# Kernel tuning notes

Measured on AMD Instinct MI355X. Metric: run time of the kernel, lower is better.

Reference implementation:

```python
import jax, jax.numpy as jnp
import numpy as np

K = 60
BATCH, NCLS, H, W = 8, 2, 512, 512


def _neighbors(x):
    # x: [B,H,W] int32 in {0,1}. Returns P2..P9 clockwise starting north.
    p = jnp.pad(x, ((0, 0), (1, 1), (1, 1)))
    P2 = p[:, :-2, 1:-1]   # N
    P3 = p[:, :-2, 2:]     # NE
    P4 = p[:, 1:-1, 2:]    # E
    P5 = p[:, 2:, 2:]      # SE
    P6 = p[:, 2:, 1:-1]    # S
    P7 = p[:, 2:, :-2]     # SW
    P8 = p[:, 1:-1, :-2]   # W
    P9 = p[:, :-2, :-2]    # NW
    return P2, P3, P4, P5, P6, P7, P8, P9


def _substep(x, first):
    # One Zhang-Suen thinning sub-iteration (the algorithm used by
    # skimage.morphology.skeletonize for 2D images).
    P2, P3, P4, P5, P6, P7, P8, P9 = _neighbors(x)
    seq = (P2, P3, P4, P5, P6, P7, P8, P9, P2)
    # A = number of 0->1 transitions in circular neighbor sequence
    A = sum(((seq[i] == 0) & (seq[i + 1] == 1)).astype(jnp.int32) for i in range(8))
    Bn = P2 + P3 + P4 + P5 + P6 + P7 + P8 + P9
    if first:
        c3 = P2 * P4 * P6
        c4 = P4 * P6 * P8
    else:
        c3 = P2 * P4 * P8
        c4 = P2 * P6 * P8
    delete = (x == 1) & (Bn >= 2) & (Bn <= 6) & (A == 1) & (c3 == 0) & (c4 == 0)
    return x * (1 - delete.astype(x.dtype))


def _skeletonize(img):
    # img: [B,H,W] int32 binary. Iterate thinning until fixed point.
    def body(state):
        x, _ = state
        x2 = _substep(_substep(x, True), False)
        return x2, jnp.any(x2 != x)

    def cond(state):
        return state[1]

    out, _ = jax.lax.while_loop(cond, body, (img, jnp.array(True)))
    return out


def _conv(x, kernel, pad):
    # x: [B,1,H,W], kernel: [1,1,k,k], 'same' padding pad
    return jax.lax.conv_general_dilated(x, kernel, (1, 1), [(pad, pad), (pad, pad)])


def setup_inputs() -> dict:
    key = jax.random.key(0)
    k1, k2 = jax.random.split(key)
    pred = jax.random.normal(k1, (BATCH, NCLS, H, W), dtype=jnp.float32)
    target = jax.random.randint(k2, (BATCH, H, W), 0, NCLS, dtype=jnp.int32)
    return {"pred": pred, "target": target}


def reference(pred, target):
    # Per-pixel cross entropy, reduction='none'
    logp = jax.nn.log_softmax(pred, axis=1)
    L = -jnp.take_along_axis(logp, target[:, None].astype(jnp.int32), axis=1)[:, 0]  # [B,H,W]

    # Skeletonize the hard prediction (nonzero = foreground)
    A = jnp.argmax(pred, axis=1)
    skel = _skeletonize((A != 0).astype(jnp.int32))  # [B,H,W]
    Bm = skel[:, None].astype(pred.dtype)            # [B,1,H,W]

    # 3x3 neighbor count (center zeroed); endpoints C where product == 1
    k3 = jnp.ones((1, 1, 3, 3), pred.dtype).at[0, 0, 1, 1].set(0.0)
    C = Bm * _conv(Bm, k3, 1)
    C = (C == 1.0).astype(pred.dtype)

    # 9x9 endpoint density, scaled by K; zeros -> weight 1
    k9 = jnp.ones((1, 1, 9, 9), pred.dtype)
    N = _conv(C, k9, 4) * K
    Wmap = N + (N == 0.0).astype(pred.dtype)  # [B,1,H,W]

    return jnp.mean(Wmap[:, 0] * L)
```

## Files before the change

### kernel.cpp

```cpp
#include <hip/hip_runtime.h>

#define BATCH   8
#define HH      512
#define WW      512
#define IMGPIX  (HH * WW)
#define NPIX    (BATCH * IMGPIX)
#define NWORDS  (NPIX / 64)
#define KFAC    60.0f
#define MAX_PAIRS 256
#define WPR     8
#define LDSTR   9
#define FPSCALE 262144.0

typedef unsigned long long u64;
typedef unsigned int u32;

__global__ void prep_kernel(const float* __restrict__ pred, const int* __restrict__ target,
                            float* __restrict__ L, u64* __restrict__ xp,
                            u64* __restrict__ acc64, u32* __restrict__ ticket) {
    int i = blockIdx.x * blockDim.x + threadIdx.x;
    if (i == 0) { acc64[0] = 0ULL; ticket[0] = 0u; }
    if (i >= NPIX) return;
    int b = i >> 18;
    int hw = i & (IMGPIX - 1);
    float p0 = pred[((size_t)(2 * b) << 18) + hw];
    float p1 = pred[((size_t)(2 * b + 1) << 18) + hw];
    float m = fmaxf(p0, p1);
    float lse = m + logf(expf(p0 - m) + expf(p1 - m));
    int t = target[i];
    L[i] = lse - (t ? p1 : p0);
    u64 word = __ballot(p1 > p0);
    if ((threadIdx.x & 63) == 0) xp[i >> 6] = word;
}

#define FA(a,b,c,s,cy) { u64 _x = (a)^(b); (s) = _x^(c); (cy) = ((a)&(b)) | ((c)&_x); }
#define HA(a,b,s,cy)   { (s) = (a)^(b); (cy) = (a)&(b); }

template<int FIRST>
__device__ __forceinline__ u32 zs_substep(u64* __restrict__ img,
                                          const u32* __restrict__ c0,
                                          const u32* __restrict__ c1,
                                          u32* __restrict__ cw, int h)
{
    u32 m = c0[h] | c1[h];
    if (h > 0)      m |= c0[h-1] | c1[h-1];
    if (h < HH-1)   m |= c0[h+1] | c1[h+1];
    u32 active = (m | (m << 1) | (m >> 1)) & 0xFFu;
    u32 loadm  = (active | (active << 1) | (active >> 1)) & 0xFFu;

    u64 U[WPR], M[WPR], D[WPR], nrow[WPR];
    #pragma unroll
    for (int wc = 0; wc < WPR; ++wc) {
        if ((loadm >> wc) & 1) {
            U[wc] = (h > 0)      ? img[(h-1) * LDSTR + wc] : 0ULL;
            M[wc] =                img[h     * LDSTR + wc];
            D[wc] = (h < HH - 1) ? img[(h+1) * LDSTR + wc] : 0ULL;
        } else { U[wc] = 0ULL; M[wc] = 0ULL; D[wc] = 0ULL; }
    }
    __syncthreads();

    u32 chnew = 0;
    #pragma unroll
    for (int wc = 0; wc < WPR; ++wc) {
        if ((active >> wc) & 1) {
            u64 Uc = U[wc], Mc = M[wc], Dc = D[wc];
            u64 Up = wc     ? U[wc-1] : 0ULL;
            u64 Mp = wc     ? M[wc-1] : 0ULL;
            u64 Dp = wc     ? D[wc-1] : 0ULL;
            u64 Un = wc < 7 ? U[wc+1] : 0ULL;
            u64 Mn = wc < 7 ? M[wc+1] : 0ULL;
            u64 Dn = wc < 7 ? D[wc+1] : 0ULL;
            u64 P2 = Uc;
            u64 P6 = Dc;
            u64 P3 = (Uc >> 1) | (Un << 63);
            u64 P4 = (Mc >> 1) | (Mn << 63);
            u64 P5 = (Dc >> 1) | (Dn << 63);
            u64 P9 = (Uc << 1) | (Up >> 63);
            u64 P8 = (Mc << 1) | (Mp >> 63);
            u64 P7 = (Dc << 1) | (Dp >> 63);

            u64 sa,ca, sb,cb, sc,cc, b0,cd, sd,ce, b1,cf, b2,b3;
            FA(P2,P3,P4, sa,ca);
            FA(P5,P6,P7, sb,cb);
            FA(P8,P9,sa, sc,cc);
            HA(sb,sc,    b0,cd);
            FA(ca,cb,cc, sd,ce);
            HA(sd,cd,    b1,cf);
            HA(ce,cf,    b2,b3);
            u64 ge2 = b1 | b2 | b3;
            u64 le6 = ~(b3 | (b0 & b1 & b2));

            u64 e, seen, two = 0;
            seen = (~P2) & P3;
            e = (~P3) & P4; two |= seen & e; seen |= e;
            e = (~P4) & P5; two |= seen & e; seen |= e;
            e = (~P5) & P6; two |= seen & e; seen |= e;
            e = (~P6) & P7; two |= seen & e; seen |= e;
            e = (~P7) & P8; two |= seen & e; seen |= e;
            e = (~P8) & P9; two |= seen & e; seen |= e;
            e = (~P9) & P2; two |= seen & e; seen |= e;
            u64 A1 = seen & ~two;

            u64 c34;
            if (FIRST) { u64 t = P4 & P6; c34 = t & (P2 | P8); }
            else       { u64 t = P2 & P8; c34 = t & (P4 | P6); }

            u64 del = Mc & ge2 & le6 & A1 & ~c34;
            nrow[wc] = Mc ^ del;
            chnew |= (u32)(del != 0ULL) << wc;
        }
    }
    #pragma unroll
    for (int wc = 0; wc < WPR; ++wc)
        if ((active >> wc) & 1) img[h * LDSTR + wc] = nrow[wc];
    cw[h] = chnew;
    return chnew;
}

__global__ __launch_bounds__(512)
void skel_kernel(const u64* __restrict__ xp, u64* __restrict__ eg)
{
    __shared__ u64 img[HH * LDSTR];
    __shared__ u32 chm[2][HH];
    const int b = blockIdx.x;
    const int h = threadIdx.x;

    const u64* src = xp + (size_t)b * (HH * WPR);
    #pragma unroll
    for (int wc = 0; wc < WPR; ++wc) img[h * LDSTR + wc] = src[h * WPR + wc];
    chm[0][h] = 0xFFu; chm[1][h] = 0xFFu;
    __syncthreads();

    for (int p = 0; p < MAX_PAIRS; ++p) {
        u32 ch1 = zs_substep<1>(img, chm[0], chm[1], chm[0], h);
        __syncthreads();
        u32 ch2 = zs_substep<0>(img, chm[0], chm[1], chm[1], h);
        if (!__syncthreads_or((ch1 | ch2) != 0)) break;
    }

    u64 U[WPR], M[WPR], D[WPR];
    #pragma unroll
    for (int wc = 0; wc < WPR; ++wc) {
        U[wc] = (h > 0)      ? img[(h-1) * LDSTR + wc] : 0ULL;
        M[wc] =                img[h     * LDSTR + wc];
        D[wc] = (h < HH - 1) ? img[(h+1) * LDSTR + wc] : 0ULL;
    }
    u64* egr = eg + (size_t)b * (HH * WPR) + (size_t)h * WPR;
    #pragma unroll
    for (int wc = 0; wc < WPR; ++wc) {
        u64 Uc = U[wc], Mc = M[wc], Dc = D[wc];
        u64 Up = wc     ? U[wc-1] : 0ULL;
        u64 Mp = wc     ? M[wc-1] : 0ULL;
        u64 Dp = wc     ? D[wc-1] : 0ULL;
        u64 Un = wc < 7 ? U[wc+1] : 0ULL;
        u64 Mn = wc < 7 ? M[wc+1] : 0ULL;
        u64 Dn = wc < 7 ? D[wc+1] : 0ULL;
        u64 P2 = Uc;
        u64 P6 = Dc;
        u64 P3 = (Uc >> 1) | (Un << 63);
        u64 P4 = (Mc >> 1) | (Mn << 63);
        u64 P5 = (Dc >> 1) | (Dn << 63);
        u64 P9 = (Uc << 1) | (Up >> 63);
        u64 P8 = (Mc << 1) | (Mp >> 63);
        u64 P7 = (Dc << 1) | (Dp >> 63);
        u64 e, seen, two = 0;
        seen = P2;
        e = P3; two |= seen & e; seen |= e;
        e = P4; two |= seen & e; seen |= e;
        e = P5; two |= seen & e; seen |= e;
        e = P6; two |= seen & e; seen |= e;
        e = P7; two |= seen & e; seen |= e;
        e = P8; two |= seen & e; seen |= e;
        e = P9; two |= seen & e; seen |= e;
        egr[wc] = Mc & seen & ~two;
    }
}

struct Planes { u64 p0, p1, p2, p3; };

__device__ __forceinline__ Planes vcount9(const u64 r[9]) {
    u64 s0,c0, s1,c1, s2,c2, p0,t0, t1,t2, p1,t3, p2,p3;
    FA(r[0],r[1],r[2], s0,c0);
    FA(r[3],r[4],r[5], s1,c1);
    FA(r[6],r[7],r[8], s2,c2);
    FA(s0,s1,s2, p0,t0);
    FA(c0,c1,c2, t1,t2);
    HA(t0,t1,    p1,t3);
    HA(t2,t3,    p2,p3);
    Planes P; P.p0 = p0; P.p1 = p1; P.p2 = p2; P.p3 = p3; return P;
}

__device__ __forceinline__ u64 spread8(u64 bb) {
    u64 s = (bb * 0x0101010101010101ULL) & 0x8040201008040201ULL;
    return ((s + 0x7f7f7f7f7f7f7f7fULL) >> 7) & 0x0101010101010101ULL;
}

__device__ __forceinline__ u64 vbytes(const Planes& P, int g) {
    int s = 8 * g;
    return  spread8((P.p0 >> s) & 0xFFULL)
         + (spread8((P.p1 >> s) & 0xFFULL) << 1)
         + (spread8((P.p2 >> s) & 0xFFULL) << 2)
         + (spread8((P.p3 >> s) & 0xFFULL) << 3);
}

__global__ __launch_bounds__(256)
void final_kernel(const float* __restrict__ L, const u64* __restrict__ eg,
                  u64* __restrict__ acc64, u32* __restrict__ ticket,
                  float* __restrict__ out) {
    __shared__ float sm[256];
    int wi = blockIdx.x * blockDim.x + threadIdx.x;
    int b  = wi >> 12;
    int h  = (wi >> 3) & (HH - 1);
    int wc = wi & 7;
    const u64* img = eg + ((size_t)b << 12);

    u64 rows[3][9];
    #pragma unroll
    for (int dh = -4; dh <= 4; ++dh) {
        int hh = h + dh;
        bool okh = (unsigned)hh < (unsigned)HH;
        const u64* rp = img + hh * WPR;
        rows[0][dh + 4] = (okh && wc > 0) ? rp[wc - 1] : 0ULL;
        rows[1][dh + 4] = okh             ? rp[wc]     : 0ULL;
        rows[2][dh + 4] = (okh && wc < 7) ? rp[wc + 1] : 0ULL;
    }
    Planes Pm = vcount9(rows[0]);
    Planes Pc = vcount9(rows[1]);
    Planes Pp = vcount9(rows[2]);

    u64 v[10];
    v[0] = vbytes(Pm, 7);
    #pragma unroll
    for (int g = 0; g < 8; ++g) v[g + 1] = vbytes(Pc, g);
    v[9] = vbytes(Pp, 0);

    const float4* Lr = (const float4*)(L + ((size_t)wi << 6));
    float acc = 0.0f;
    #pragma unroll
    for (int g = 0; g < 8; ++g) {
        u64 a = v[g + 1], lo = v[g], hi = v[g + 2];
        u64 n = a;
        #pragma unroll
        for (int d = 1; d <= 4; ++d) {
            n += (a >> (8 * d)) | (hi << (64 - 8 * d));
            n += (a << (8 * d)) | (lo >> (64 - 8 * d));
        }
        float4 f0 = Lr[2 * g], f1 = Lr[2 * g + 1];
        #pragma unroll
        for (int j = 0; j < 8; ++j) {
            int cnt = (int)((n >> (8 * j)) & 0xFFULL);
            float wgt = cnt ? (float)(60 * cnt) : 1.0f;
            float lv = (j < 4) ? ((j == 0) ? f0.x : (j == 1) ? f0.y : (j == 2) ? f0.z : f0.w)
                               : ((j == 4) ? f1.x : (j == 5) ? f1.y : (j == 6) ? f1.z : f1.w);
            acc += wgt * lv;
        }
    }

    sm[threadIdx.x] = acc;
    __syncthreads();
    for (int s = 128; s > 0; s >>= 1) {
        if (threadIdx.x < s) sm[threadIdx.x] += sm[threadIdx.x + s];
        __syncthreads();
    }
    if (threadIdx.x == 0) {
        u64 vfx = (u64)(long long)llrintf(sm[0] * (float)FPSCALE);
        atomicAdd(acc64, vfx);
        __threadfence();
        u32 t = atomicAdd(ticket, 1u);
        if (t == (u32)(gridDim.x - 1)) {
            __threadfence();
            u64 total = __hip_atomic_load(acc64, __ATOMIC_RELAXED, __HIP_MEMORY_SCOPE_AGENT);
            out[0] = (float)((double)(long long)total / (FPSCALE * (double)NPIX));
        }
    }
}

extern "C" void kernel_launch(void* const* d_in, const int* in_sizes, int n_in,
                              void* d_out, int out_size, void* d_ws, size_t ws_size,
                              hipStream_t stream) {
    const float* pred = (const float*)d_in[0];
    const int* target = (const int*)d_in[1];
    float* out = (float*)d_out;
    char* ws = (char*)d_ws;

    float* L    = (float*)(ws);
    u64* xp     = (u64*)(ws + 8388608);
    u64* eg     = (u64*)(ws + 8650752);
    u64* acc64  = (u64*)(ws + 8912896);
    u32* ticket = (u32*)(ws + 8912904);

    prep_kernel<<<dim3(NPIX / 256), dim3(256), 0, stream>>>(pred, target, L, xp, acc64, ticket);
    skel_kernel<<<dim3(BATCH), dim3(512), 0, stream>>>(xp, eg);
    final_kernel<<<dim3(NWORDS / 256), dim3(256), 0, stream>>>(L, eg, acc64, ticket, out);
}
```

Before: 62.01 us.

## Keep own skeleton row in registers with padded LDS halo rows

Rewrites the thinning loop so each thread keeps its own row in registers and only reloads the neighbouring rows from LDS. It adds zero halo rows so boundary checks disappear. It drops the per-row change-mask activity tracking and instead skips all-zero words and skips the LDS writeback when nothing changed. This trades the earlier sparse-activity skipping for fewer LDS loads, simpler control flow and lower register pressure. Words with foreground but no changes are now always recomputed.

```diff
diff --git a/kernel.cpp b/kernel.cpp
--- a/kernel.cpp
+++ b/kernel.cpp
@@ -6,11 +6,10 @@
 #define IMGPIX  (HH * WW)
 #define NPIX    (BATCH * IMGPIX)
 #define NWORDS  (NPIX / 64)
-#define KFAC    60.0f
-#define MAX_PAIRS 256
 #define WPR     8
 #define LDSTR   9
 #define FPSCALE 262144.0
+#define MAXPAIR 256
 
 typedef unsigned long long u64;
 typedef unsigned int u32;
@@ -37,126 +36,117 @@
 #define HA(a,b,s,cy)   { (s) = (a)^(b); (cy) = (a)&(b); }
 
 template<int FIRST>
-__device__ __forceinline__ u32 zs_substep(u64* __restrict__ img,
-                                          const u32* __restrict__ c0,
-                                          const u32* __restrict__ c1,
-                                          u32* __restrict__ cw, int h)
+__device__ __forceinline__ u64 zs_row(const u64* __restrict__ U, u64* __restrict__ M,
+                                      const u64* __restrict__ D)
 {
-    u32 m = c0[h] | c1[h];
-    if (h > 0)      m |= c0[h-1] | c1[h-1];
-    if (h < HH-1)   m |= c0[h+1] | c1[h+1];
-    u32 active = (m | (m << 1) | (m >> 1)) & 0xFFu;
-    u32 loadm  = (active | (active << 1) | (active >> 1)) & 0xFFu;
-
-    u64 U[WPR], M[WPR], D[WPR], nrow[WPR];
-    #pragma unroll
-    for (int wc = 0; wc < WPR; ++wc) {
-        if ((loadm >> wc) & 1) {
-            U[wc] = (h > 0)      ? img[(h-1) * LDSTR + wc] : 0ULL;
-            M[wc] =                img[h     * LDSTR + wc];
-            D[wc] = (h < HH - 1) ? img[(h+1) * LDSTR + wc] : 0ULL;
-        } else { U[wc] = 0ULL; M[wc] = 0ULL; D[wc] = 0ULL; }
-    }
-    __syncthreads();
-
-    u32 chnew = 0;
-    #pragma unroll
-    for (int wc = 0; wc < WPR; ++wc) {
-        if ((active >> wc) & 1) {
-            u64 Uc = U[wc], Mc = M[wc], Dc = D[wc];
-            u64 Up = wc     ? U[wc-1] : 0ULL;
-            u64 Mp = wc     ? M[wc-1] : 0ULL;
-            u64 Dp = wc     ? D[wc-1] : 0ULL;
-            u64 Un = wc < 7 ? U[wc+1] : 0ULL;
-            u64 Mn = wc < 7 ? M[wc+1] : 0ULL;
-            u64 Dn = wc < 7 ? D[wc+1] : 0ULL;
-            u64 P2 = Uc;
-            u64 P6 = Dc;
-            u64 P3 = (Uc >> 1) | (Un << 63);
-            u64 P4 = (Mc >> 1) | (Mn << 63);
-            u64 P5 = (Dc >> 1) | (Dn << 63);
-            u64 P9 = (Uc << 1) | (Up >> 63);
-            u64 P8 = (Mc << 1) | (Mp >> 63);
-            u64 P7 = (Dc << 1) | (Dp >> 63);
-
-            u64 sa,ca, sb,cb, sc,cc, b0,cd, sd,ce, b1,cf, b2,b3;
-            FA(P2,P3,P4, sa,ca);
-            FA(P5,P6,P7, sb,cb);
-            FA(P8,P9,sa, sc,cc);
-            HA(sb,sc,    b0,cd);
-            FA(ca,cb,cc, sd,ce);
-            HA(sd,cd,    b1,cf);
-            HA(ce,cf,    b2,b3);
-            u64 ge2 = b1 | b2 | b3;
-            u64 le6 = ~(b3 | (b0 & b1 & b2));
-
-            u64 e, seen, two = 0;
-            seen = (~P2) & P3;
-            e = (~P3) & P4; two |= seen & e; seen |= e;
-            e = (~P4) & P5; two |= seen & e; seen |= e;
-            e = (~P5) & P6; two |= seen & e; seen |= e;
-            e = (~P6) & P7; two |= seen & e; seen |= e;
-            e = (~P7) & P8; two |= seen & e; seen |= e;
-            e = (~P8) & P9; two |= seen & e; seen |= e;
-            e = (~P9) & P2; two |= seen & e; seen |= e;
-            u64 A1 = seen & ~two;
-
-            u64 c34;
-            if (FIRST) { u64 t = P4 & P6; c34 = t & (P2 | P8); }
-            else       { u64 t = P2 & P8; c34 = t & (P4 | P6); }
-
-            u64 del = Mc & ge2 & le6 & A1 & ~c34;
-            nrow[wc] = Mc ^ del;
-            chnew |= (u32)(del != 0ULL) << wc;
-        }
-    }
-    #pragma unroll
-    for (int wc = 0; wc < WPR; ++wc)
-        if ((active >> wc) & 1) img[h * LDSTR + wc] = nrow[wc];
-    cw[h] = chnew;
-    return chnew;
+    u64 ch = 0;
+    #pragma unroll
+    for (int k = 0; k < WPR; ++k) {
+        u64 Mc = M[k];
+        if (Mc == 0ULL) continue;
+        u64 Uc = U[k], Dc = D[k];
+        u64 Up = k     ? U[k-1] : 0ULL;
+        u64 Mp = k     ? M[k-1] : 0ULL;
+        u64 Dp = k     ? D[k-1] : 0ULL;
+        u64 Un = k < 7 ? U[k+1] : 0ULL;
+        u64 Mn = k < 7 ? M[k+1] : 0ULL;
+        u64 Dn = k < 7 ? D[k+1] : 0ULL;
+        u64 P2 = Uc, P6 = Dc;
+        u64 P3 = (Uc >> 1) | (Un << 63);
+        u64 P4 = (Mc >> 1) | (Mn << 63);
+        u64 P5 = (Dc >> 1) | (Dn << 63);
+        u64 P9 = (Uc << 1) | (Up >> 63);
+        u64 P8 = (Mc << 1) | (Mp >> 63);
+        u64 P7 = (Dc << 1) | (Dp >> 63);
+
+        u64 sa,ca, sb,cb, sc,cc, b0,cd, sd,ce, b1,cf, b2,b3;
+        FA(P2,P3,P4, sa,ca);
+        FA(P5,P6,P7, sb,cb);
+        FA(P8,P9,sa, sc,cc);
+        HA(sb,sc,    b0,cd);
+        FA(ca,cb,cc, sd,ce);
+        HA(sd,cd,    b1,cf);
+        HA(ce,cf,    b2,b3);
+        u64 ge2 = b1 | b2 | b3;
+        u64 le6 = ~(b3 | (b0 & b1 & b2));
+
+        u64 e, seen, two = 0;
+        seen = (~P2) & P3;
+        e = (~P3) & P4; two |= seen & e; seen |= e;
+        e = (~P4) & P5; two |= seen & e; seen |= e;
+        e = (~P5) & P6; two |= seen & e; seen |= e;
+        e = (~P6) & P7; two |= seen & e; seen |= e;
+        e = (~P7) & P8; two |= seen & e; seen |= e;
+        e = (~P8) & P9; two |= seen & e; seen |= e;
+        e = (~P9) & P2; two |= seen & e; seen |= e;
+        u64 A1 = seen & ~two;
+
+        u64 c34;
+        if (FIRST) { u64 t = P4 & P6; c34 = t & (P2 | P8); }
+        else       { u64 t = P2 & P8; c34 = t & (P4 | P6); }
+
+        u64 del = Mc & ge2 & le6 & A1 & ~c34;
+        M[k] = Mc ^ del;
+        ch |= del;
+    }
+    return ch;
 }
 
 __global__ __launch_bounds__(512)
 void skel_kernel(const u64* __restrict__ xp, u64* __restrict__ eg)
 {
-    __shared__ u64 img[HH * LDSTR];
-    __shared__ u32 chm[2][HH];
+    __shared__ u64 img[(HH + 2) * LDSTR];
     const int b = blockIdx.x;
     const int h = threadIdx.x;
-
-    const u64* src = xp + (size_t)b * (HH * WPR);
-    #pragma unroll
-    for (int wc = 0; wc < WPR; ++wc) img[h * LDSTR + wc] = src[h * WPR + wc];
-    chm[0][h] = 0xFFu; chm[1][h] = 0xFFu;
+    const int base = (h + 1) * LDSTR;
+
+    if (h < 2 * LDSTR) {
+        int idx = (h < LDSTR) ? h : ((HH + 1) * LDSTR + (h - LDSTR));
+        img[idx] = 0ULL;
+    }
+
+    u64 M[WPR], U[WPR], D[WPR];
+    const u64* src = xp + ((size_t)b << 12) + (size_t)h * WPR;
+    #pragma unroll
+    for (int k = 0; k < WPR; ++k) { M[k] = src[k]; img[base + k] = M[k]; }
     __syncthreads();
 
-    for (int p = 0; p < MAX_PAIRS; ++p) {
-        u32 ch1 = zs_substep<1>(img, chm[0], chm[1], chm[0], h);
-        __syncthreads();
-        u32 ch2 = zs_substep<0>(img, chm[0], chm[1], chm[1], h);
-        if (!__syncthreads_or((ch1 | ch2) != 0)) break;
-    }
-
-    u64 U[WPR], M[WPR], D[WPR];
-    #pragma unroll
-    for (int wc = 0; wc < WPR; ++wc) {
-        U[wc] = (h > 0)      ? img[(h-1) * LDSTR + wc] : 0ULL;
-        M[wc] =                img[h     * LDSTR + wc];
-        D[wc] = (h < HH - 1) ? img[(h+1) * LDSTR + wc] : 0ULL;
-    }
-    u64* egr = eg + (size_t)b * (HH * WPR) + (size_t)h * WPR;
-    #pragma unroll
-    for (int wc = 0; wc < WPR; ++wc) {
-        u64 Uc = U[wc], Mc = M[wc], Dc = D[wc];
-        u64 Up = wc     ? U[wc-1] : 0ULL;
-        u64 Mp = wc     ? M[wc-1] : 0ULL;
-        u64 Dp = wc     ? D[wc-1] : 0ULL;
-        u64 Un = wc < 7 ? U[wc+1] : 0ULL;
-        u64 Mn = wc < 7 ? M[wc+1] : 0ULL;
-        u64 Dn = wc < 7 ? D[wc+1] : 0ULL;
-        u64 P2 = Uc;
-        u64 P6 = Dc;
+    for (int p = 0; p < MAXPAIR; ++p) {
+        #pragma unroll
+        for (int k = 0; k < WPR; ++k) { U[k] = img[base - LDSTR + k]; D[k] = img[base + LDSTR + k]; }
+        __syncthreads();
+        u64 chA = zs_row<1>(U, M, D);
+        if (chA) {
+            #pragma unroll
+            for (int k = 0; k < WPR; ++k) img[base + k] = M[k];
+        }
+        __syncthreads();
+
+        #pragma unroll
+        for (int k = 0; k < WPR; ++k) { U[k] = img[base - LDSTR + k]; D[k] = img[base + LDSTR + k]; }
+        __syncthreads();
+        u64 chB = zs_row<0>(U, M, D);
+        if (chB) {
+            #pragma unroll
+            for (int k = 0; k < WPR; ++k) img[base + k] = M[k];
+        }
+        if (!__syncthreads_or((chA | chB) != 0ULL)) break;
+    }
+
+    #pragma unroll
+    for (int k = 0; k < WPR; ++k) { U[k] = img[base - LDSTR + k]; D[k] = img[base + LDSTR + k]; }
+    u64* egr = eg + ((size_t)b << 12) + (size_t)h * WPR;
+    #pragma unroll
+    for (int k = 0; k < WPR; ++k) {
+        u64 Mc = M[k];
+        u64 Uc = U[k], Dc = D[k];
+        u64 Up = k     ? U[k-1] : 0ULL;
+        u64 Mp = k     ? M[k-1] : 0ULL;
+        u64 Dp = k     ? D[k-1] : 0ULL;
+        u64 Un = k < 7 ? U[k+1] : 0ULL;
+        u64 Mn = k < 7 ? M[k+1] : 0ULL;
+        u64 Dn = k < 7 ? D[k+1] : 0ULL;
+        u64 P2 = Uc, P6 = Dc;
         u64 P3 = (Uc >> 1) | (Un << 63);
         u64 P4 = (Mc >> 1) | (Mn << 63);
         u64 P5 = (Dc >> 1) | (Dn << 63);
@@ -172,7 +162,7 @@
         e = P7; two |= seen & e; seen |= e;
         e = P8; two |= seen & e; seen |= e;
         e = P9; two |= seen & e; seen |= e;
-        egr[wc] = Mc & seen & ~two;
+        egr[k] = Mc & seen & ~two;
     }
 }
 
```

After: 61.77 us. Within noise of the previous version (-0.4%).
